# Kernel optimization log

Measured on AMD Instinct MI355X. Metric: run time of the kernel, lower is better.

Reference implementation:

```python
import jax, jax.numpy as jnp
import numpy as np

D = 1024
H = 16
HD = D // H  # 64
B = 2
T = 2048


def setup_inputs() -> dict:
    key = jax.random.key(0)
    ks = jax.random.split(key, 5)
    s = 0.02
    return {
        "x": jax.random.normal(ks[0], (B, T, D), dtype=jnp.float32),
        "Wqkv": jax.random.normal(ks[1], (D, 3 * H * HD), dtype=jnp.float32) * s,
        "bqkv": jnp.zeros((3 * H * HD,), dtype=jnp.float32),
        "Wout": jax.random.normal(ks[2], (H * HD, D), dtype=jnp.float32) * s,
        "bout": jnp.zeros((D,), dtype=jnp.float32),
    }


def reference(x, Wqkv, bqkv, Wout, bout):
    b, t, _ = x.shape
    qkv = (x @ Wqkv + bqkv).reshape(b, t, 3, H, HD)
    q, k, v = qkv[:, :, 0], qkv[:, :, 1], qkv[:, :, 2]  # [b,t,h,hd]
    sc = jnp.einsum("bqhd,bkhd->bhqk", q, k) / jnp.sqrt(jnp.float32(HD))
    attn = jax.nn.softmax(sc, axis=-1)
    ctx = jnp.einsum("bhqk,bkhd->bqhd", attn, v).reshape(b, t, H * HD)
    return ctx @ Wout + bout
```

## Files before the change

### kernel.cpp

```cpp
#include <hip/hip_runtime.h>
#include <hip/hip_bf16.h>


typedef __attribute__((ext_vector_type(8))) short bf16x8;
typedef __attribute__((ext_vector_type(4))) float f32x4;

__device__ __forceinline__ short f2b(float f) {
    __hip_bfloat16 h = __float2bfloat16(f);
    union { __hip_bfloat16 h; short s; } u; u.h = h;
    return u.s;
}

#define GLOAD_LDS16(gp, lp)                                                        \
    __builtin_amdgcn_global_load_lds(                                              \
        (const __attribute__((address_space(1))) unsigned int*)(gp),               \
        (__attribute__((address_space(3))) unsigned int*)(lp), 16, 0, 0)

__global__ __launch_bounds__(256) void xcvt_kernel(
    const float* __restrict__ in, short* __restrict__ out) {
    const int i = (blockIdx.x * 256 + threadIdx.x) * 8;
    float4 v0 = *reinterpret_cast<const float4*>(in + i);
    float4 v1 = *reinterpret_cast<const float4*>(in + i + 4);
    union { short s[8]; uint4 q; } pk;
    pk.s[0] = f2b(v0.x); pk.s[1] = f2b(v0.y); pk.s[2] = f2b(v0.z); pk.s[3] = f2b(v0.w);
    pk.s[4] = f2b(v1.x); pk.s[5] = f2b(v1.y); pk.s[6] = f2b(v1.z); pk.s[7] = f2b(v1.w);
    *reinterpret_cast<uint4*>(out + i) = pk.q;
}

__global__ __launch_bounds__(256) void transpose_w_kernel(
    const float* __restrict__ in, short* __restrict__ out, int R, int C) {
    __shared__ short lds[64][72];
    const int t = threadIdx.x;
    const int r0 = blockIdx.y * 64, c0 = blockIdx.x * 64;
    {
        const int ri = t >> 2, cb = (t & 3) * 16;
        const float* src = in + (size_t)(r0 + ri) * C + c0 + cb;
#pragma unroll
        for (int i = 0; i < 16; i += 4) {
            float4 v = *reinterpret_cast<const float4*>(src + i);
            lds[cb + i + 0][ri] = f2b(v.x);
            lds[cb + i + 1][ri] = f2b(v.y);
            lds[cb + i + 2][ri] = f2b(v.z);
            lds[cb + i + 3][ri] = f2b(v.w);
        }
    }
    __syncthreads();
    {
        const int co = t >> 2, rb = (t & 3) * 16;
        short* dst = out + (size_t)(c0 + co) * R + r0 + rb;
        *reinterpret_cast<uint4*>(dst)     = *reinterpret_cast<const uint4*>(&lds[co][rb]);
        *reinterpret_cast<uint4*>(dst + 8) = *reinterpret_cast<const uint4*>(&lds[co][rb + 8]);
    }
}

__global__ __launch_bounds__(256) void gemm1_kernel(
    const short* __restrict__ XB, const short* __restrict__ WT,
    const float* __restrict__ bqkv,
    short* __restrict__ qb, short* __restrict__ kb, short* __restrict__ vtb) {
    __shared__ short a_lds[2][128 * 32];
    __shared__ short b_lds[2][128 * 32];
    const int tid = threadIdx.x;
    const int lane = tid & 63, w = tid >> 6;
    const int wr = w >> 1, wc = w & 1;
    const int m0 = blockIdx.y * 128, n0 = blockIdx.x * 128;
    f32x4 acc[4][4] = {};

    const int srow0 = tid >> 2, ssl = tid & 3;
    const int slc0 = (ssl ^ ((srow0 >> 1) & 3)) * 8;
    const int srow1 = srow0 + 64;
    const int slc1 = (ssl ^ ((srow1 >> 1) & 3)) * 8;

#define G1_STAGE(bufi, kk)                                                          \
    do {                                                                            \
        GLOAD_LDS16(XB + (size_t)(m0 + srow0) * 1024 + (kk) + slc0,                 \
                    &a_lds[bufi][(w * 64) * 8]);                                    \
        GLOAD_LDS16(WT + (size_t)(n0 + srow0) * 1024 + (kk) + slc0,                 \
                    &b_lds[bufi][(w * 64) * 8]);                                    \
        GLOAD_LDS16(XB + (size_t)(m0 + srow1) * 1024 + (kk) + slc1,                 \
                    &a_lds[bufi][(256 + w * 64) * 8]);                              \
        GLOAD_LDS16(WT + (size_t)(n0 + srow1) * 1024 + (kk) + slc1,                 \
                    &b_lds[bufi][(256 + w * 64) * 8]);                              \
    } while (0)

    G1_STAGE(0, 0);
    __syncthreads();
    int cur = 0;
    for (int k0 = 0; k0 < 1024; k0 += 32) {
        if (k0 + 32 < 1024) G1_STAGE(cur ^ 1, k0 + 32);
        bf16x8 af[4], bfv[4];
#pragma unroll
        for (int mi = 0; mi < 4; ++mi) {
            const int rA = wr * 64 + mi * 16 + (lane & 15);
            const int sl = (lane >> 4) ^ ((rA >> 1) & 3);
            af[mi] = *reinterpret_cast<const bf16x8*>(&a_lds[cur][rA * 32 + sl * 8]);
        }
#pragma unroll
        for (int nj = 0; nj < 4; ++nj) {
            const int rB = wc * 64 + nj * 16 + (lane & 15);
            const int sl = (lane >> 4) ^ ((rB >> 1) & 3);
            bfv[nj] = *reinterpret_cast<const bf16x8*>(&b_lds[cur][rB * 32 + sl * 8]);
        }
#pragma unroll
        for (int mi = 0; mi < 4; ++mi)
#pragma unroll
            for (int nj = 0; nj < 4; ++nj)
                acc[mi][nj] = __builtin_amdgcn_mfma_f32_16x16x32_bf16(af[mi], bfv[nj], acc[mi][nj], 0, 0, 0);
        __syncthreads();
        cur ^= 1;
    }

    const float QSCL = 0.125f * 1.44269504088896340736f;
#pragma unroll
    for (int mi = 0; mi < 4; ++mi) {
#pragma unroll
        for (int nj = 0; nj < 4; ++nj) {
            const int row0 = m0 + wr * 64 + mi * 16 + ((lane >> 4) << 2);
            const int col  = n0 + wc * 64 + nj * 16 + (lane & 15);
            const float bias = bqkv[col];
            const int sec = col >> 10;
            const int h = (col & 1023) >> 6, d = col & 63;
            const int b = row0 >> 11;
            const int bh = b * 16 + h;
            if (sec == 2) {
                const int t0 = row0 & 2047;
                union { short s[4]; uint2 u; } pk;
#pragma unroll
                for (int r = 0; r < 4; ++r) pk.s[r] = f2b(acc[mi][nj][r] + bias);
                *reinterpret_cast<uint2*>(vtb + (size_t)(bh * 64 + d) * 2048 + t0) = pk.u;
            } else if (sec == 0) {
#pragma unroll
                for (int r = 0; r < 4; ++r) {
                    const int t = (row0 & 2047) + r;
                    qb[(size_t)(bh * 2048 + t) * 64 + d] = f2b((acc[mi][nj][r] + bias) * QSCL);
                }
            } else {
#pragma unroll
                for (int r = 0; r < 4; ++r) {
                    const int t = (row0 & 2047) + r;
                    kb[(size_t)(bh * 2048 + t) * 64 + d] = f2b(acc[mi][nj][r] + bias);
                }
            }
        }
    }
}

__global__ __launch_bounds__(512) void attn_kernel(
    const short* __restrict__ qb, const short* __restrict__ kb,
    const short* __restrict__ vtb, short* __restrict__ ctx) {
    __shared__ short k_lds[2][64 * 64];
    __shared__ short v_lds[2][64 * 64];
    __shared__ short p_lds[8][16][68];
    const int tid = threadIdx.x, lane = tid & 63, w = tid >> 6;
    const int g = lane >> 4, qh = lane & 15;
    const int h = blockIdx.y, b = blockIdx.z, bh = b * 16 + h;
    const int qbase = blockIdx.x * 128;
    const int tq = qbase + w * 16 + qh;

    bf16x8 qf[2];
#pragma unroll
    for (int ks = 0; ks < 2; ++ks)
        qf[ks] = *reinterpret_cast<const bf16x8*>(
            qb + (size_t)(bh * 2048 + tq) * 64 + ks * 32 + g * 8);

    const int srow = tid >> 3, ssl = tid & 7;
    const int slc = (ssl ^ (srow & 7)) * 8;

#define ATT_STAGE(bufi, kv)                                                         \
    do {                                                                            \
        GLOAD_LDS16(kb + (size_t)(bh * 2048 + (kv) + srow) * 64 + slc,              \
                    &k_lds[bufi][w * 512]);                                         \
        GLOAD_LDS16(vtb + (size_t)(bh * 64 + srow) * 2048 + (kv) + slc,             \
                    &v_lds[bufi][w * 512]);                                         \
    } while (0)

    f32x4 o[4] = {};
    float m_s = -1e30f, l_s = 0.f;

    ATT_STAGE(0, 0);
    __syncthreads();
    int cur = 0;
    for (int kv0 = 0; kv0 < 2048; kv0 += 64) {
        if (kv0 + 64 < 2048) ATT_STAGE(cur ^ 1, kv0 + 64);

        f32x4 s[4] = {};
#pragma unroll
        for (int ks = 0; ks < 2; ++ks)
#pragma unroll
            for (int nt = 0; nt < 4; ++nt) {
                const int rK = nt * 16 + qh;
                const int sl = (ks * 4 + g) ^ (rK & 7);
                bf16x8 kf = *reinterpret_cast<const bf16x8*>(&k_lds[cur][rK * 64 + sl * 8]);
                s[nt] = __builtin_amdgcn_mfma_f32_16x16x32_bf16(kf, qf[ks], s[nt], 0, 0, 0);
            }

        float mx = s[0][0];
#pragma unroll
        for (int nt = 0; nt < 4; ++nt)
#pragma unroll
            for (int r = 0; r < 4; ++r) mx = fmaxf(mx, s[nt][r]);
        mx = fmaxf(mx, __shfl_xor(mx, 16));
        mx = fmaxf(mx, __shfl_xor(mx, 32));
        const float mn = fmaxf(m_s, mx);
        if (__any(mn - m_s > 8.f)) {
            const float alpha = exp2f(m_s - mn);
            m_s = mn;
            l_s *= alpha;
#pragma unroll
            for (int r = 0; r < 4; ++r) {
                const float ar = __shfl(alpha, g * 4 + r);
                o[0][r] *= ar; o[1][r] *= ar; o[2][r] *= ar; o[3][r] *= ar;
            }
        }

        float rs = 0.f;
#pragma unroll
        for (int nt = 0; nt < 4; ++nt) {
            union { short s4[4]; uint2 u; } P;
#pragma unroll
            for (int r = 0; r < 4; ++r) {
                const float p = exp2f(s[nt][r] - m_s);
                rs += p;
                P.s4[r] = f2b(p);
            }
            *reinterpret_cast<uint2*>(&p_lds[w][qh][nt * 16 + 4 * g]) = P.u;
        }
        rs += __shfl_xor(rs, 16);
        rs += __shfl_xor(rs, 32);
        l_s += rs;

#pragma unroll
        for (int ks2 = 0; ks2 < 2; ++ks2) {
            bf16x8 pa = *reinterpret_cast<const bf16x8*>(&p_lds[w][qh][ks2 * 32 + g * 8]);
#pragma unroll
            for (int nt = 0; nt < 4; ++nt) {
                const int rV = nt * 16 + qh;
                const int sl = (ks2 * 4 + g) ^ (rV & 7);
                bf16x8 vf = *reinterpret_cast<const bf16x8*>(&v_lds[cur][rV * 64 + sl * 8]);
                o[nt] = __builtin_amdgcn_mfma_f32_16x16x32_bf16(pa, vf, o[nt], 0, 0, 0);
            }
        }
        __syncthreads();
        cur ^= 1;
    }

#pragma unroll
    for (int r = 0; r < 4; ++r) {
        const float linv = 1.0f / __shfl(l_s, g * 4 + r);
        const int trow = qbase + w * 16 + g * 4 + r;
#pragma unroll
        for (int nt = 0; nt < 4; ++nt)
            ctx[(size_t)(b * 2048 + trow) * 1024 + h * 64 + nt * 16 + qh] =
                f2b(o[nt][r] * linv);
    }
}

__global__ __launch_bounds__(256) void gemm2_kernel(
    const short* __restrict__ CTX, const short* __restrict__ WT,
    const float* __restrict__ bout, float* __restrict__ out) {
    __shared__ short a_lds[2][128 * 32];
    __shared__ short b_lds[2][128 * 32];
    const int tid = threadIdx.x;
    const int lane = tid & 63, w = tid >> 6;
    const int wr = w >> 1, wc = w & 1;
    const int m0 = blockIdx.y * 128, n0 = blockIdx.x * 128;
    f32x4 acc[4][4] = {};

    const int srow0 = tid >> 2, ssl = tid & 3;
    const int slc0 = (ssl ^ ((srow0 >> 1) & 3)) * 8;
    const int srow1 = srow0 + 64;
    const int slc1 = (ssl ^ ((srow1 >> 1) & 3)) * 8;

#define G2_STAGE(bufi, kk)                                                          \
    do {                                                                            \
        GLOAD_LDS16(CTX + (size_t)(m0 + srow0) * 1024 + (kk) + slc0,                \
                    &a_lds[bufi][(w * 64) * 8]);                                    \
        GLOAD_LDS16(WT + (size_t)(n0 + srow0) * 1024 + (kk) + slc0,                 \
                    &b_lds[bufi][(w * 64) * 8]);                                    \
        GLOAD_LDS16(CTX + (size_t)(m0 + srow1) * 1024 + (kk) + slc1,                \
                    &a_lds[bufi][(256 + w * 64) * 8]);                              \
        GLOAD_LDS16(WT + (size_t)(n0 + srow1) * 1024 + (kk) + slc1,                 \
                    &b_lds[bufi][(256 + w * 64) * 8]);                              \
    } while (0)

    G2_STAGE(0, 0);
    __syncthreads();
    int cur = 0;
    for (int k0 = 0; k0 < 1024; k0 += 32) {
        if (k0 + 32 < 1024) G2_STAGE(cur ^ 1, k0 + 32);
        bf16x8 af[4], bfv[4];
#pragma unroll
        for (int mi = 0; mi < 4; ++mi) {
            const int rA = wr * 64 + mi * 16 + (lane & 15);
            const int sl = (lane >> 4) ^ ((rA >> 1) & 3);
            af[mi] = *reinterpret_cast<const bf16x8*>(&a_lds[cur][rA * 32 + sl * 8]);
        }
#pragma unroll
        for (int nj = 0; nj < 4; ++nj) {
            const int rB = wc * 64 + nj * 16 + (lane & 15);
            const int sl = (lane >> 4) ^ ((rB >> 1) & 3);
            bfv[nj] = *reinterpret_cast<const bf16x8*>(&b_lds[cur][rB * 32 + sl * 8]);
        }
#pragma unroll
        for (int mi = 0; mi < 4; ++mi)
#pragma unroll
            for (int nj = 0; nj < 4; ++nj)
                acc[mi][nj] = __builtin_amdgcn_mfma_f32_16x16x32_bf16(af[mi], bfv[nj], acc[mi][nj], 0, 0, 0);
        __syncthreads();
        cur ^= 1;
    }

#pragma unroll
    for (int mi = 0; mi < 4; ++mi) {
#pragma unroll
        for (int nj = 0; nj < 4; ++nj) {
            const int row0 = m0 + wr * 64 + mi * 16 + ((lane >> 4) << 2);
            const int col  = n0 + wc * 64 + nj * 16 + (lane & 15);
            const float bias = bout[col];
#pragma unroll
            for (int r = 0; r < 4; ++r)
                out[(size_t)(row0 + r) * 1024 + col] = acc[mi][nj][r] + bias;
        }
    }
}

extern "C" void kernel_launch(void* const* d_in, const int* in_sizes, int n_in,
                              void* d_out, int out_size, void* d_ws, size_t ws_size,
                              hipStream_t stream) {
    const float* x    = (const float*)d_in[0];
    const float* Wqkv = (const float*)d_in[1];
    const float* bqkv = (const float*)d_in[2];
    const float* Wout = (const float*)d_in[3];
    const float* bout = (const float*)d_in[4];
    float* out = (float*)d_out;

    const size_t MB = 1u << 20;
    if (ws_size < 40 * MB) return;

    char* ws = (char*)d_ws;
    short* qb    = (short*)(ws + 0 * MB);
    short* kb    = (short*)(ws + 8 * MB);
    short* vtb   = (short*)(ws + 16 * MB);
    short* xbctx = (short*)(ws + 24 * MB);
    short* wqkvT = (short*)(ws + 32 * MB);
    short* woutT = (short*)(ws + 38 * MB);

    xcvt_kernel<<<2048, 256, 0, stream>>>(x, xbctx);
    transpose_w_kernel<<<dim3(48, 16), 256, 0, stream>>>(Wqkv, wqkvT, 1024, 3072);
    transpose_w_kernel<<<dim3(16, 16), 256, 0, stream>>>(Wout, woutT, 1024, 1024);
    gemm1_kernel<<<dim3(24, 32), 256, 0, stream>>>(xbctx, wqkvT, bqkv, qb, kb, vtb);
    attn_kernel<<<dim3(16, 16, 2), 512, 0, stream>>>(qb, kb, vtb, xbctx);
    gemm2_kernel<<<dim3(8, 32), 256, 0, stream>>>(xbctx, woutT, bout, out);
}
```

Before: 215.8 us.

## Use 32x32 MFMA attention with in-register P via permlane swap and XCD swizzle

The attention kernel switches from 16x16x32 to 32x32x16 bf16 MFMA, with 4 waves per block each owning 32 queries. The P matrix stays in registers: it is packed with v_cvt_pk_bf16_f32 and rearranged with v_permlane32_swap, which removes the LDS round trip and some shuffles. exp2 now uses the hardware builtin. Both GEMMs and the attention grid remap block indices so blocks sharing data land on the same XCD for L2 reuse. The risk is the larger accumulator footprint (32 floats for O), which may reduce occupancy.

```diff
diff --git a/kernel.cpp b/kernel.cpp
--- a/kernel.cpp
+++ b/kernel.cpp
@@ -4,6 +4,13 @@
 
 typedef __attribute__((ext_vector_type(8))) short bf16x8;
 typedef __attribute__((ext_vector_type(4))) float f32x4;
+typedef __attribute__((ext_vector_type(16))) float f32x16;
+
+#if __has_builtin(__builtin_amdgcn_exp2f)
+#define EXP2(x) __builtin_amdgcn_exp2f(x)
+#else
+#define EXP2(x) exp2f(x)
+#endif
 
 __device__ __forceinline__ short f2b(float f) {
     __hip_bfloat16 h = __float2bfloat16(f);
@@ -62,7 +69,9 @@
     const int tid = threadIdx.x;
     const int lane = tid & 63, w = tid >> 6;
     const int wr = w >> 1, wc = w & 1;
-    const int m0 = blockIdx.y * 128, n0 = blockIdx.x * 128;
+    const int lin = blockIdx.x + 24 * blockIdx.y;
+    const int swz = (lin & 7) * 96 + (lin >> 3);
+    const int m0 = (swz / 24) * 128, n0 = (swz % 24) * 128;
     f32x4 acc[4][4] = {};
 
     const int srow0 = tid >> 2, ssl = tid & 3;
@@ -144,36 +153,46 @@
     }
 }
 
-__global__ __launch_bounds__(512) void attn_kernel(
+__global__ __launch_bounds__(256) void attn_kernel(
     const short* __restrict__ qb, const short* __restrict__ kb,
     const short* __restrict__ vtb, short* __restrict__ ctx) {
     __shared__ short k_lds[2][64 * 64];
     __shared__ short v_lds[2][64 * 64];
-    __shared__ short p_lds[8][16][68];
     const int tid = threadIdx.x, lane = tid & 63, w = tid >> 6;
-    const int g = lane >> 4, qh = lane & 15;
-    const int h = blockIdx.y, b = blockIdx.z, bh = b * 16 + h;
-    const int qbase = blockIdx.x * 128;
-    const int tq = qbase + w * 16 + qh;
-
-    bf16x8 qf[2];
-#pragma unroll
-    for (int ks = 0; ks < 2; ++ks)
-        qf[ks] = *reinterpret_cast<const bf16x8*>(
-            qb + (size_t)(bh * 2048 + tq) * 64 + ks * 32 + g * 8);
-
-    const int srow = tid >> 3, ssl = tid & 7;
-    const int slc = (ssl ^ (srow & 7)) * 8;
+    const int q31 = lane & 31, hi = lane >> 5;
+
+    const int dlin = blockIdx.x + 16 * (blockIdx.y + 16 * blockIdx.z);
+    const int xcd = dlin & 7, ii = dlin >> 3;
+    const int bh = xcd * 4 + (ii >> 4);
+    const int qblk = ii & 15;
+    const int b = bh >> 4, h = bh & 15;
+    const int tq = qblk * 128 + w * 32 + q31;
+
+    bf16x8 qf[4];
+#pragma unroll
+    for (int s = 0; s < 4; ++s)
+        qf[s] = *reinterpret_cast<const bf16x8*>(
+            qb + (size_t)(bh * 2048 + tq) * 64 + s * 16 + hi * 8);
+
+    const int srow_l = lane >> 3, ssl = lane & 7;
+    const int row_a = w * 8 + srow_l;
+    const int row_b = 32 + w * 8 + srow_l;
+    const int lc_a = (ssl ^ (row_a & 7)) * 8;
+    const int lc_b = (ssl ^ (row_b & 7)) * 8;
 
 #define ATT_STAGE(bufi, kv)                                                         \
     do {                                                                            \
-        GLOAD_LDS16(kb + (size_t)(bh * 2048 + (kv) + srow) * 64 + slc,              \
-                    &k_lds[bufi][w * 512]);                                         \
-        GLOAD_LDS16(vtb + (size_t)(bh * 64 + srow) * 2048 + (kv) + slc,             \
-                    &v_lds[bufi][w * 512]);                                         \
+        GLOAD_LDS16(kb + (size_t)(bh * 2048 + (kv) + row_a) * 64 + lc_a,            \
+                    &k_lds[bufi][(w * 8) * 64]);                                    \
+        GLOAD_LDS16(vtb + (size_t)(bh * 64 + row_a) * 2048 + (kv) + lc_a,           \
+                    &v_lds[bufi][(w * 8) * 64]);                                    \
+        GLOAD_LDS16(kb + (size_t)(bh * 2048 + (kv) + row_b) * 64 + lc_b,            \
+                    &k_lds[bufi][(32 * 64) + (w * 8) * 64]);                        \
+        GLOAD_LDS16(vtb + (size_t)(bh * 64 + row_b) * 2048 + (kv) + lc_b,           \
+                    &v_lds[bufi][(32 * 64) + (w * 8) * 64]);                        \
     } while (0)
 
-    f32x4 o[4] = {};
+    f32x16 o0 = {}, o1 = {};
     float m_s = -1e30f, l_s = 0.f;
 
     ATT_STAGE(0, 0);
@@ -182,75 +201,97 @@
     for (int kv0 = 0; kv0 < 2048; kv0 += 64) {
         if (kv0 + 64 < 2048) ATT_STAGE(cur ^ 1, kv0 + 64);
 
-        f32x4 s[4] = {};
-#pragma unroll
-        for (int ks = 0; ks < 2; ++ks)
-#pragma unroll
-            for (int nt = 0; nt < 4; ++nt) {
-                const int rK = nt * 16 + qh;
-                const int sl = (ks * 4 + g) ^ (rK & 7);
-                bf16x8 kf = *reinterpret_cast<const bf16x8*>(&k_lds[cur][rK * 64 + sl * 8]);
-                s[nt] = __builtin_amdgcn_mfma_f32_16x16x32_bf16(kf, qf[ks], s[nt], 0, 0, 0);
-            }
-
-        float mx = s[0][0];
-#pragma unroll
-        for (int nt = 0; nt < 4; ++nt)
-#pragma unroll
-            for (int r = 0; r < 4; ++r) mx = fmaxf(mx, s[nt][r]);
-        mx = fmaxf(mx, __shfl_xor(mx, 16));
+        f32x16 sA0 = {}, sA1 = {};
+#pragma unroll
+        for (int s = 0; s < 4; ++s) {
+            {
+                const int row = q31;
+                const int sl = (2 * s + hi) ^ (row & 7);
+                bf16x8 kf = *reinterpret_cast<const bf16x8*>(&k_lds[cur][row * 64 + sl * 8]);
+                sA0 = __builtin_amdgcn_mfma_f32_32x32x16_bf16(kf, qf[s], sA0, 0, 0, 0);
+            }
+            {
+                const int row = 32 + q31;
+                const int sl = (2 * s + hi) ^ (row & 7);
+                bf16x8 kf = *reinterpret_cast<const bf16x8*>(&k_lds[cur][row * 64 + sl * 8]);
+                sA1 = __builtin_amdgcn_mfma_f32_32x32x16_bf16(kf, qf[s], sA1, 0, 0, 0);
+            }
+        }
+
+        float mA[8];
+#pragma unroll
+        for (int e = 0; e < 8; ++e)
+            mA[e] = fmaxf(fmaxf(sA0[e], sA0[e + 8]), fmaxf(sA1[e], sA1[e + 8]));
+        float mx = fmaxf(fmaxf(fmaxf(mA[0], mA[1]), fmaxf(mA[2], mA[3])),
+                         fmaxf(fmaxf(mA[4], mA[5]), fmaxf(mA[6], mA[7])));
         mx = fmaxf(mx, __shfl_xor(mx, 32));
+
         const float mn = fmaxf(m_s, mx);
         if (__any(mn - m_s > 8.f)) {
-            const float alpha = exp2f(m_s - mn);
+            const float alpha = EXP2(m_s - mn);
             m_s = mn;
             l_s *= alpha;
 #pragma unroll
-            for (int r = 0; r < 4; ++r) {
-                const float ar = __shfl(alpha, g * 4 + r);
-                o[0][r] *= ar; o[1][r] *= ar; o[2][r] *= ar; o[3][r] *= ar;
-            }
+            for (int e = 0; e < 16; ++e) { o0[e] *= alpha; o1[e] *= alpha; }
         }
 
         float rs = 0.f;
-#pragma unroll
-        for (int nt = 0; nt < 4; ++nt) {
-            union { short s4[4]; uint2 u; } P;
-#pragma unroll
-            for (int r = 0; r < 4; ++r) {
-                const float p = exp2f(s[nt][r] - m_s);
-                rs += p;
-                P.s4[r] = f2b(p);
-            }
-            *reinterpret_cast<uint2*>(&p_lds[w][qh][nt * 16 + 4 * g]) = P.u;
-        }
-        rs += __shfl_xor(rs, 16);
+        int W0[8], W1[8];
+#pragma unroll
+        for (int m2 = 0; m2 < 8; ++m2) {
+            float p0 = EXP2(sA0[2 * m2] - m_s);
+            float p1 = EXP2(sA0[2 * m2 + 1] - m_s);
+            rs += p0 + p1;
+            asm("v_cvt_pk_bf16_f32 %0, %1, %2" : "=v"(W0[m2]) : "v"(p0), "v"(p1));
+            float p2 = EXP2(sA1[2 * m2] - m_s);
+            float p3 = EXP2(sA1[2 * m2 + 1] - m_s);
+            rs += p2 + p3;
+            asm("v_cvt_pk_bf16_f32 %0, %1, %2" : "=v"(W1[m2]) : "v"(p2), "v"(p3));
+        }
         rs += __shfl_xor(rs, 32);
         l_s += rs;
 
 #pragma unroll
-        for (int ks2 = 0; ks2 < 2; ++ks2) {
-            bf16x8 pa = *reinterpret_cast<const bf16x8*>(&p_lds[w][qh][ks2 * 32 + g * 8]);
-#pragma unroll
-            for (int nt = 0; nt < 4; ++nt) {
-                const int rV = nt * 16 + qh;
-                const int sl = (ks2 * 4 + g) ^ (rV & 7);
-                bf16x8 vf = *reinterpret_cast<const bf16x8*>(&v_lds[cur][rV * 64 + sl * 8]);
-                o[nt] = __builtin_amdgcn_mfma_f32_16x16x32_bf16(pa, vf, o[nt], 0, 0, 0);
+        for (int s = 0; s < 4; ++s) {
+            const int base = (s & 1) * 4;
+            int x0, x1, y0, y1;
+            if (s < 2) { x0 = W0[base]; x1 = W0[base + 1]; y0 = W0[base + 2]; y1 = W0[base + 3]; }
+            else       { x0 = W1[base]; x1 = W1[base + 1]; y0 = W1[base + 2]; y1 = W1[base + 3]; }
+            asm("v_permlane32_swap_b32 %0, %1" : "+v"(x0), "+v"(y0));
+            asm("v_permlane32_swap_b32 %0, %1" : "+v"(x1), "+v"(y1));
+            union { int w[4]; bf16x8 v; } pf;
+            pf.w[0] = x0; pf.w[1] = x1; pf.w[2] = y0; pf.w[3] = y1;
+            {
+                const int row = q31;
+                const int sl = (2 * s + hi) ^ (row & 7);
+                bf16x8 vf = *reinterpret_cast<const bf16x8*>(&v_lds[cur][row * 64 + sl * 8]);
+                o0 = __builtin_amdgcn_mfma_f32_32x32x16_bf16(vf, pf.v, o0, 0, 0, 0);
+            }
+            {
+                const int row = 32 + q31;
+                const int sl = (2 * s + hi) ^ (row & 7);
+                bf16x8 vf = *reinterpret_cast<const bf16x8*>(&v_lds[cur][row * 64 + sl * 8]);
+                o1 = __builtin_amdgcn_mfma_f32_32x32x16_bf16(vf, pf.v, o1, 0, 0, 0);
             }
         }
         __syncthreads();
         cur ^= 1;
     }
 
-#pragma unroll
-    for (int r = 0; r < 4; ++r) {
-        const float linv = 1.0f / __shfl(l_s, g * 4 + r);
-        const int trow = qbase + w * 16 + g * 4 + r;
-#pragma unroll
-        for (int nt = 0; nt < 4; ++nt)
-            ctx[(size_t)(b * 2048 + trow) * 1024 + h * 64 + nt * 16 + qh] =
-                f2b(o[nt][r] * linv);
+    const float linv = 1.0f / l_s;
+#pragma unroll
+    for (int e = 0; e < 16; ++e) { o0[e] *= linv; o1[e] *= linv; }
+    short* cbase = ctx + (size_t)(b * 2048 + tq) * 1024 + h * 64 + 4 * hi;
+#pragma unroll
+    for (int blk = 0; blk < 4; ++blk) {
+        union { short s4[4]; uint2 u; } pk0, pk1;
+#pragma unroll
+        for (int r = 0; r < 4; ++r) {
+            pk0.s4[r] = f2b(o0[4 * blk + r]);
+            pk1.s4[r] = f2b(o1[4 * blk + r]);
+        }
+        *reinterpret_cast<uint2*>(cbase + 8 * blk)      = pk0.u;
+        *reinterpret_cast<uint2*>(cbase + 32 + 8 * blk) = pk1.u;
     }
 }
 
@@ -262,7 +303,9 @@
     const int tid = threadIdx.x;
     const int lane = tid & 63, w = tid >> 6;
     const int wr = w >> 1, wc = w & 1;
-    const int m0 = blockIdx.y * 128, n0 = blockIdx.x * 128;
+    const int lin = blockIdx.x + 8 * blockIdx.y;
+    const int swz = (lin & 7) * 32 + (lin >> 3);
+    const int m0 = (swz >> 3) * 128, n0 = (swz & 7) * 128;
     f32x4 acc[4][4] = {};
 
     const int srow0 = tid >> 2, ssl = tid & 3;
@@ -348,6 +391,6 @@
     transpose_w_kernel<<<dim3(48, 16), 256, 0, stream>>>(Wqkv, wqkvT, 1024, 3072);
     transpose_w_kernel<<<dim3(16, 16), 256, 0, stream>>>(Wout, woutT, 1024, 1024);
     gemm1_kernel<<<dim3(24, 32), 256, 0, stream>>>(xbctx, wqkvT, bqkv, qb, kb, vtb);
-    attn_kernel<<<dim3(16, 16, 2), 512, 0, stream>>>(qb, kb, vtb, xbctx);
+    attn_kernel<<<dim3(16, 16, 2), 256, 0, stream>>>(qb, kb, vtb, xbctx);
     gemm2_kernel<<<dim3(8, 32), 256, 0, stream>>>(xbctx, woutT, bout, out);
 }
```

Measured after the change: 198.1 us. 1.09x faster.
